# Kernel tuning notes

Hardware: AMD Instinct MI355X
Metric: run time of the kernel (lower is better)

## Reference

```python
import jax, jax.numpy as jnp
import numpy as np

B, D_IN, E, H, V = 4096, 4096, 2048, 2048, 32000


def setup_inputs() -> dict:
    key = jax.random.key(0)
    ks = jax.random.split(key, 24)
    s = 0.02
    p = lambda k, shape: (jax.random.normal(k, shape, dtype=jnp.float32) * s)
    return {
        "input": jax.random.normal(ks[0], (B, D_IN), dtype=jnp.float32),
        "hidden": jnp.zeros((B, H), dtype=jnp.float32),
        "cell": jnp.zeros((B, H), dtype=jnp.float32),
        # embedding linear (input_size -> emb_size), stored as [in, out]
        "We": p(ks[1], (D_IN, E)), "be": p(ks[2], (E,)),
        # x-to-gate linears (emb -> hidden)
        "Wf": p(ks[3], (E, H)), "bf": p(ks[4], (H,)),
        "Wi": p(ks[5], (E, H)), "bi": p(ks[6], (H,)),
        "Wc": p(ks[7], (E, H)), "bc": p(ks[8], (H,)),
        "Wo": p(ks[9], (E, H)), "bo": p(ks[10], (H,)),
        # hidden-to-gate linears (hidden -> hidden)
        "Uf": p(ks[11], (H, H)), "bhf": p(ks[12], (H,)),
        "Ui": p(ks[13], (H, H)), "bhi": p(ks[14], (H,)),
        "Uc": p(ks[15], (H, H)), "bhc": p(ks[16], (H,)),
        "Uo": p(ks[17], (H, H)), "bho": p(ks[18], (H,)),
        # output head (hidden -> output_size)
        "Wend": p(ks[19], (H, V)), "bend": p(ks[20], (V,)),
    }


def reference(input, hidden, cell,
              We, be, Wf, bf, Wi, bi, Wc, bc, Wo, bo,
              Uf, bhf, Ui, bhi, Uc, bhc, Uo, bho, Wend, bend):
    # embedded = Linear(input)
    emb = input @ We + be                                  # [B, E]
    f = jax.nn.sigmoid(emb @ Wf + bf + hidden @ Uf + bhf)  # forget gate [B, H]
    i = jax.nn.sigmoid(emb @ Wi + bi + hidden @ Ui + bhi)  # input gate
    g = jnp.tanh(emb @ Wc + bc + hidden @ Uc + bhc)        # candidate cell
    new_cell = f * cell + i * g
    o = jax.nn.sigmoid(emb @ Wo + bo + hidden @ Uo + bho)  # output gate
    new_hidden = o * jnp.tanh(new_cell)
    out = jax.nn.log_softmax(new_hidden @ Wend + bend, axis=1)  # [B, V]
    return (out, new_hidden, new_cell)
```

## Files before the change

### kernel.cpp

```cpp
#include <hip/hip_runtime.h>
#include <stdint.h>

#define B_DIM 4096
#define DIN   4096
#define E_DIM 2048
#define H_DIM 2048
#define V_DIM 32000

typedef __attribute__((ext_vector_type(8))) short s8v;
typedef __attribute__((ext_vector_type(4))) float f4v;
typedef __attribute__((ext_vector_type(4))) int   i4v;
typedef __attribute__((ext_vector_type(8))) int   i8v;
typedef __attribute__((ext_vector_type(16))) float f16v;

__device__ __forceinline__ ushort f2bf(float f) {
    union { float f; uint32_t u; } v; v.f = f;
    uint32_t u = v.u;
    return (ushort)((u + 0x7FFFu + ((u >> 16) & 1u)) >> 16);
}

__device__ __forceinline__ uint8_t f2fp8(float x) {
    union { float f; uint32_t u; } v; v.f = x;
    uint8_t sign = (uint8_t)((v.u >> 24) & 0x80u);
    uint32_t a = v.u & 0x7FFFFFFFu;
    if (a >= 0x43E00000u) return sign | 0x7E;
    uint32_t r = a + 0x0007FFFFu + ((a >> 20) & 1u);
    int e = (int)(r >> 23) - 127 + 7;
    if (e <= 0) {
        float s = fabsf(x);
        int q = (int)(s * 512.0f + 0.5f);
        if (q > 7) q = 7;
        return sign | (uint8_t)q;
    }
    uint32_t m = (r >> 20) & 7u;
    uint8_t b = (uint8_t)((e << 3) | m);
    if (b == 0x7F) b = 0x7E;
    return sign | b;
}

__global__ void k_cvt(const float* __restrict__ src, ushort* __restrict__ dst, int n4) {
    int i = blockIdx.x * blockDim.x + threadIdx.x;
    if (i >= n4) return;
    float4 v = *(const float4*)(src + (size_t)i * 4);
    ushort4 o;
    o.x = f2bf(v.x); o.y = f2bf(v.y); o.z = f2bf(v.z); o.w = f2bf(v.w);
    *(ushort4*)(dst + (size_t)i * 4) = o;
}

__global__ void k_cvt_hidden(const float* __restrict__ src, ushort* __restrict__ dst) {
    int i = blockIdx.x * blockDim.x + threadIdx.x;
    int b = i >> 9;
    int c = (i & 511) << 2;
    float4 v = *(const float4*)(src + (size_t)b * H_DIM + c);
    ushort4 o;
    o.x = f2bf(v.x); o.y = f2bf(v.y); o.z = f2bf(v.z); o.w = f2bf(v.w);
    *(ushort4*)(dst + (size_t)b * 4096 + 2048 + c) = o;
}

__global__ void k_transpose_bf16(const float* __restrict__ src, ushort* __restrict__ dst,
                                 int srcCols, int dstStride, int dstRowOff, int dstColOff) {
    __shared__ float tile[32][33];
    int tx = threadIdx.x, ty = threadIdx.y;
    int n0 = blockIdx.x * 32, k0 = blockIdx.y * 32;
#pragma unroll
    for (int i = 0; i < 4; i++)
        tile[ty + 8 * i][tx] = src[(size_t)(k0 + ty + 8 * i) * srcCols + n0 + tx];
    __syncthreads();
#pragma unroll
    for (int i = 0; i < 4; i++) {
        int n = ty + 8 * i;
        dst[(size_t)(dstRowOff + n0 + n) * dstStride + dstColOff + k0 + tx] = f2bf(tile[tx][n]);
    }
}

__global__ void k_transpose_fp8(const float* __restrict__ src, uint8_t* __restrict__ dst,
                                int srcCols, int dstStride) {
    __shared__ float tile[32][33];
    int tx = threadIdx.x, ty = threadIdx.y;
    int n0 = blockIdx.x * 32, k0 = blockIdx.y * 32;
#pragma unroll
    for (int i = 0; i < 4; i++)
        tile[ty + 8 * i][tx] = src[(size_t)(k0 + ty + 8 * i) * srcCols + n0 + tx];
    __syncthreads();
#pragma unroll
    for (int i = 0; i < 4; i++) {
        int n = ty + 8 * i;
        dst[(size_t)(n0 + n) * dstStride + k0 + tx] = f2fp8(tile[tx][n] * 32.0f);
    }
}

__global__ void k_transpose_gate(const float* __restrict__ src, ushort* __restrict__ dst,
                                 int g, int dstColOff) {
    __shared__ float tile[32][33];
    int tx = threadIdx.x, ty = threadIdx.y;
    int n0 = blockIdx.x * 32, k0 = blockIdx.y * 32;
#pragma unroll
    for (int i = 0; i < 4; i++)
        tile[ty + 8 * i][tx] = src[(size_t)(k0 + ty + 8 * i) * H_DIM + n0 + tx];
    __syncthreads();
#pragma unroll
    for (int i = 0; i < 4; i++) {
        int h = n0 + ty + 8 * i;
        int drow = ((h >> 6) << 8) + ((g >> 1) << 7) + (((h >> 4) & 3) << 5) + ((g & 1) << 4) + (h & 15);
        dst[(size_t)drow * 4096 + dstColOff + k0 + tx] = f2bf(tile[tx][ty + 8 * i]);
    }
}

__global__ void k_biaspack(const float* __restrict__ b0, const float* __restrict__ bh0,
                           const float* __restrict__ b1, const float* __restrict__ bh1,
                           const float* __restrict__ b2, const float* __restrict__ bh2,
                           const float* __restrict__ b3, const float* __restrict__ bh3,
                           float* __restrict__ out) {
    int h = blockIdx.x * blockDim.x + threadIdx.x;
    if (h >= H_DIM) return;
    int base = ((h >> 6) << 8) + (((h >> 4) & 3) << 5) + (h & 15);
    out[base]             = b0[h] + bh0[h];
    out[base + 16]        = b1[h] + bh1[h];
    out[base + 128]       = b2[h] + bh2[h];
    out[base + 128 + 16]  = b3[h] + bh3[h];
}

template<int OUT_BF16>
__global__ __launch_bounds__(256, 2)
void k_gemm_bt(const ushort* __restrict__ A, const ushort* __restrict__ Bt,
               void* __restrict__ Cv, const float* __restrict__ bias,
               int M, int N, int K, int lda, int ldb, int ldc) {
    __shared__ __align__(16) ushort ldsA[128 * 64];
    __shared__ __align__(16) ushort ldsB[128 * 64];
    const int t = threadIdx.x;
    const int wid = t >> 6, lane = t & 63;

    int nwg = gridDim.x;
    int bid = blockIdx.x;
    int wg  = (bid & 7) * (nwg >> 3) + (bid >> 3);
    int NT  = N >> 7;
    int mt  = wg / NT, nt = wg - mt * NT;
    int m0  = mt << 7, n0 = nt << 7;

    f4v acc[4][4];
#pragma unroll
    for (int i = 0; i < 4; i++)
#pragma unroll
        for (int j = 0; j < 4; j++) acc[i][j] = (f4v){0.f, 0.f, 0.f, 0.f};

    const int wr = wid >> 1, wc = wid & 1;

    const int kTiles = K >> 6;
    for (int kt = 0; kt < kTiles; ++kt) {
#pragma unroll
        for (int c = 0; c < 4; ++c) {
            int idx = c * 256 + wid * 64 + lane;
            int row = idx >> 3;
            int kb  = (idx & 7) << 4;
            const ushort* gA = A  + (size_t)(m0 + row) * lda + (kt << 6) + (kb >> 1);
            const ushort* gB = Bt + (size_t)(n0 + row) * ldb + (kt << 6) + (kb >> 1);
            char* lA = (char*)ldsA + (size_t)(c * 256 + wid * 64) * 16;
            char* lB = (char*)ldsB + (size_t)(c * 256 + wid * 64) * 16;
            __builtin_amdgcn_global_load_lds((const __attribute__((address_space(1))) void*)gA,
                                             (__attribute__((address_space(3))) void*)lA, 16, 0, 0);
            __builtin_amdgcn_global_load_lds((const __attribute__((address_space(1))) void*)gB,
                                             (__attribute__((address_space(3))) void*)lB, 16, 0, 0);
        }
        __syncthreads();

#pragma unroll
        for (int ks = 0; ks < 2; ++ks) {
            s8v af[4], bfr[4];
#pragma unroll
            for (int m = 0; m < 4; ++m) {
                int r = wr * 64 + m * 16 + (lane & 15);
                int kb = ks * 64 + ((lane >> 4) << 4);
                af[m] = *(const s8v*)((const char*)ldsA + r * 128 + kb);
            }
#pragma unroll
            for (int n = 0; n < 4; ++n) {
                int r = wc * 64 + n * 16 + (lane & 15);
                int kb = ks * 64 + ((lane >> 4) << 4);
                bfr[n] = *(const s8v*)((const char*)ldsB + r * 128 + kb);
            }
#pragma unroll
            for (int m = 0; m < 4; ++m)
#pragma unroll
                for (int n = 0; n < 4; ++n)
                    acc[m][n] = __builtin_amdgcn_mfma_f32_16x16x32_bf16(af[m], bfr[n], acc[m][n], 0, 0, 0);
        }
        __syncthreads();
    }

#pragma unroll
    for (int n = 0; n < 4; ++n) {
        int cg = n0 + wc * 64 + n * 16 + (lane & 15);
        float bv = bias[cg];
#pragma unroll
        for (int m = 0; m < 4; ++m) {
            int rbase = m0 + wr * 64 + m * 16 + ((lane >> 4) << 2);
#pragma unroll
            for (int r = 0; r < 4; ++r) {
                float v = acc[m][n][r] + bv;
                if (OUT_BF16)
                    ((ushort*)Cv)[(size_t)(rbase + r) * ldc + cg] = f2bf(v);
                else
                    ((float*)Cv)[(size_t)(rbase + r) * ldc + cg] = v;
            }
        }
    }
}

template<int EPI>
__global__ __launch_bounds__(512, 2)
void k_gemm256(const ushort* __restrict__ A, const ushort* __restrict__ Bt,
               void* __restrict__ Cv, const float* __restrict__ bias,
               int N, int K, int lda, int ldb, int ldc,
               const float* __restrict__ cell, float* __restrict__ outH,
               float* __restrict__ outC, uint8_t* __restrict__ hidF8,
               float2* __restrict__ partials, int ncb) {
    __shared__ __align__(16) ushort ldsA[2][256 * 64];
    __shared__ __align__(16) ushort ldsB[2][256 * 64];
    const int t = threadIdx.x;
    const int wid = t >> 6, lane = t & 63;
    const int wr = wid >> 2, wc = wid & 3;

    int nwg = gridDim.x, bid = blockIdx.x;
    int wg = (bid & 7) * (nwg >> 3) + (bid >> 3);
    int NT = N >> 8;
    int mt = wg / NT, nt = wg - mt * NT;
    int m0 = mt << 8, n0 = nt << 8;

    int offA[4], offB[4];
#pragma unroll
    for (int cc = 0; cc < 4; ++cc) {
        int idx = cc * 512 + t;
        int row = idx >> 3;
        int col = ((idx & 7) ^ (row & 7)) << 3;
        offA[cc] = (m0 + row) * lda + col;
        offB[cc] = (n0 + row) * ldb + col;
    }

#define GLOAD(GP, LP) __builtin_amdgcn_global_load_lds(                                   \
        (const __attribute__((address_space(1))) void*)(GP),                              \
        (__attribute__((address_space(3))) void*)(LP), 16, 0, 0)
#define STAGE_HA(BUF, KT, H) do {                                                         \
    GLOAD(A + offA[(H)*2]     + ((KT) << 6), &ldsA[BUF][(((H)*2)*512 + (wid<<6)) * 8]);   \
    GLOAD(A + offA[(H)*2 + 1] + ((KT) << 6), &ldsA[BUF][(((H)*2+1)*512 + (wid<<6)) * 8]); \
} while (0)
#define STAGE_HB(BUF, KT, H) do {                                                         \
    GLOAD(Bt + offB[(H)*2]     + ((KT) << 6), &ldsB[BUF][(((H)*2)*512 + (wid<<6)) * 8]);  \
    GLOAD(Bt + offB[(H)*2 + 1] + ((KT) << 6), &ldsB[BUF][(((H)*2+1)*512 + (wid<<6)) * 8]);\
} while (0)

    f4v acc[8][4];
#pragma unroll
    for (int i = 0; i < 8; i++)
#pragma unroll
        for (int j = 0; j < 4; j++) acc[i][j] = (f4v){0.f, 0.f, 0.f, 0.f};

    s8v af[4][2], bfA[2][2], bfB[2][2];
    const int swz = (lane & 7) << 4;
    const int kcol = (lane >> 4) << 4;

#define READ_A(BUF, MH) do {                                                              \
    _Pragma("unroll")                                                                     \
    for (int m_ = 0; m_ < 4; ++m_) {                                                      \
        int row = (MH)*128 + wr*64 + m_*16 + (lane & 15);                                 \
        _Pragma("unroll")                                                                 \
        for (int ks_ = 0; ks_ < 2; ++ks_)                                                 \
            af[m_][ks_] = *(const s8v*)((const char*)&ldsA[BUF][0] + row * 128 +          \
                                        ((ks_*64 + kcol) ^ swz));                         \
    } } while (0)
#define READ_B(BUF, NH, DST) do {                                                         \
    _Pragma("unroll")                                                                     \
    for (int n_ = 0; n_ < 2; ++n_) {                                                      \
        int row = (NH)*128 + wc*32 + n_*16 + (lane & 15);                                 \
        _Pragma("unroll")                                                                 \
        for (int ks_ = 0; ks_ < 2; ++ks_)                                                 \
            DST[n_][ks_] = *(const s8v*)((const char*)&ldsB[BUF][0] + row * 128 +         \
                                         ((ks_*64 + kcol) ^ swz));                        \
    } } while (0)
#define MFMA_Q(MH, NH, BF) do {                                                           \
    __builtin_amdgcn_s_setprio(1);                                                        \
    _Pragma("unroll")                                                                     \
    for (int m_ = 0; m_ < 4; ++m_)                                                        \
    _Pragma("unroll")                                                                     \
    for (int n_ = 0; n_ < 2; ++n_)                                                        \
    _Pragma("unroll")                                                                     \
    for (int ks_ = 0; ks_ < 2; ++ks_)                                                     \
        acc[(MH)*4 + m_][(NH)*2 + n_] = __builtin_amdgcn_mfma_f32_16x16x32_bf16(          \
            af[m_][ks_], BF[n_][ks_], acc[(MH)*4 + m_][(NH)*2 + n_], 0, 0, 0);            \
    __builtin_amdgcn_s_setprio(0);                                                        \
} while (0)
#define MEMBAR asm volatile("" ::: "memory")
#define BAR() do { MEMBAR; __builtin_amdgcn_s_barrier(); MEMBAR; } while (0)
#define WAITLGKM0() do { asm volatile("s_waitcnt lgkmcnt(0)" ::: "memory");               \
                         __builtin_amdgcn_sched_barrier(0); } while (0)

    const int kTiles = K >> 6;
    STAGE_HA(0, 0, 0); STAGE_HB(0, 0, 0); STAGE_HB(0, 0, 1); STAGE_HA(0, 0, 1);
    STAGE_HA(1, 1, 0); STAGE_HB(1, 1, 0); STAGE_HB(1, 1, 1); STAGE_HA(1, 1, 1);
    asm volatile("s_waitcnt vmcnt(6)" ::: "memory");
    BAR();

    for (int kt = 0; kt < kTiles; ++kt) {
        const int buf = kt & 1;
        const bool pf = (kt + 2 < kTiles);
        READ_A(buf, 0); READ_B(buf, 0, bfA);
        asm volatile("s_waitcnt lgkmcnt(8)" ::: "memory");
        BAR(); WAITLGKM0();
        MFMA_Q(0, 0, bfA);
        BAR();
        READ_B(buf, 1, bfB);
        if (pf) STAGE_HA(buf, kt + 2, 0);
        BAR(); WAITLGKM0();
        MFMA_Q(0, 1, bfB);
        BAR();
        READ_A(buf, 1);
        if (pf) STAGE_HB(buf, kt + 2, 0);
        BAR(); WAITLGKM0();
        MFMA_Q(1, 1, bfB);
        BAR();
        if (pf) { STAGE_HB(buf, kt + 2, 1); STAGE_HA(buf, kt + 2, 1); }
        MFMA_Q(1, 0, bfA);
        if (pf) asm volatile("s_waitcnt vmcnt(8)" ::: "memory");
        else    asm volatile("s_waitcnt vmcnt(0)" ::: "memory");
        BAR();
    }

    if (EPI == 0) {
    } else {
        int h = (n0 >> 2) + wc * 16 + (lane & 15);
        float bv[4];
#pragma unroll
        for (int j = 0; j < 4; ++j)
            bv[j] = bias[n0 + (j >> 1) * 128 + wc * 32 + (j & 1) * 16 + (lane & 15)];
#pragma unroll
        for (int mh = 0; mh < 2; ++mh)
#pragma unroll
        for (int m = 0; m < 4; ++m) {
            int rb = m0 + mh * 128 + wr * 64 + m * 16 + ((lane >> 4) << 2);
#pragma unroll
            for (int r = 0; r < 4; ++r) {
                int b = rb + r;
                float pf_ = acc[mh * 4 + m][0][r] + bv[0];
                float pi_ = acc[mh * 4 + m][1][r] + bv[1];
                float pc_ = acc[mh * 4 + m][2][r] + bv[2];
                float po_ = acc[mh * 4 + m][3][r] + bv[3];
                float fg = 1.f / (1.f + __expf(-pf_));
                float ig = 1.f / (1.f + __expf(-pi_));
                float gg = tanhf(pc_);
                float og = 1.f / (1.f + __expf(-po_));
                size_t off = (size_t)b * H_DIM + h;
                float nc = fg * cell[off] + ig * gg;
                float nh = og * tanhf(nc);
                outC[off] = nc;
                outH[off] = nh;
                hidF8[off] = f2fp8(nh * 8.0f);
            }
        }
    }
#undef GLOAD
#undef STAGE_HA
#undef STAGE_HB
#undef READ_A
#undef READ_B
#undef MFMA_Q
#undef MEMBAR
#undef BAR
#undef WAITLGKM0
}

__global__ __launch_bounds__(256, 3)
void k_gemm_mx(const uint8_t* __restrict__ A, const uint8_t* __restrict__ Bt,
               float* __restrict__ C, const float* __restrict__ bias,
               float2* __restrict__ partials, int N, int K, int ldc, int ncb) {
    __shared__ __align__(16) uint8_t ldsA[128 * 128];
    __shared__ __align__(16) uint8_t ldsB[128 * 128];
    const int t = threadIdx.x;
    const int wid = t >> 6, lane = t & 63;
    const int wrr = wid >> 1, wcc = wid & 1;

    int nwg = gridDim.x, bid = blockIdx.x;
    int wg = (bid & 7) * (nwg >> 3) + (bid >> 3);
    int NT = N >> 7;
    int mt = wg / NT, nt = wg - mt * NT;
    int m0 = mt << 7, n0 = nt << 7;

    int offA[4], offB[4];
#pragma unroll
    for (int c = 0; c < 4; ++c) {
        int idx = c * 256 + t;
        int row = idx >> 3;
        int cb  = ((idx & 7) ^ (row & 7)) << 4;
        offA[c] = (m0 + row) * K + cb;
        offB[c] = (n0 + row) * K + cb;
    }

    f16v acc[2][2];
#pragma unroll
    for (int i = 0; i < 2; ++i)
#pragma unroll
        for (int j = 0; j < 2; ++j)
#pragma unroll
            for (int r = 0; r < 16; ++r) acc[i][j][r] = 0.f;

    const int lr32 = lane & 31;
    const int kh   = (lane >> 5) << 5;

    const int kTiles = K >> 7;
    for (int kt = 0; kt < kTiles; ++kt) {
#pragma unroll
        for (int c = 0; c < 4; ++c) {
            __builtin_amdgcn_global_load_lds(
                (const __attribute__((address_space(1))) void*)(A + offA[c] + (kt << 7)),
                (__attribute__((address_space(3))) void*)&ldsA[(c * 256 + wid * 64) * 16], 16, 0, 0);
            __builtin_amdgcn_global_load_lds(
                (const __attribute__((address_space(1))) void*)(Bt + offB[c] + (kt << 7)),
                (__attribute__((address_space(3))) void*)&ldsB[(c * 256 + wid * 64) * 16], 16, 0, 0);
        }
        __syncthreads();

#pragma unroll
        for (int kk = 0; kk < 2; ++kk) {
            i8v af[2], bf[2];
#pragma unroll
            for (int mi = 0; mi < 2; ++mi) {
                int row = wrr * 64 + mi * 32 + lr32;
                int sw = (row & 7) << 4;
                int o0 = (kk * 64 + kh) ^ sw;
                int o1 = (kk * 64 + kh + 16) ^ sw;
                i4v lo = *(const i4v*)&ldsA[row * 128 + o0];
                i4v hi = *(const i4v*)&ldsA[row * 128 + o1];
                af[mi] = __builtin_shufflevector(lo, hi, 0, 1, 2, 3, 4, 5, 6, 7);
            }
#pragma unroll
            for (int ni = 0; ni < 2; ++ni) {
                int row = wcc * 64 + ni * 32 + lr32;
                int sw = (row & 7) << 4;
                int o0 = (kk * 64 + kh) ^ sw;
                int o1 = (kk * 64 + kh + 16) ^ sw;
                i4v lo = *(const i4v*)&ldsB[row * 128 + o0];
                i4v hi = *(const i4v*)&ldsB[row * 128 + o1];
                bf[ni] = __builtin_shufflevector(lo, hi, 0, 1, 2, 3, 4, 5, 6, 7);
            }
#pragma unroll
            for (int mi = 0; mi < 2; ++mi)
#pragma unroll
                for (int ni = 0; ni < 2; ++ni)
                    acc[mi][ni] = __builtin_amdgcn_mfma_scale_f32_32x32x64_f8f6f4(
                        af[mi], bf[ni], acc[mi][ni], 0, 0, 0, 124, 0, 122);
        }
        __syncthreads();
    }

    float bv[2];
    int cg0 = n0 + wcc * 64 + lr32;
    bv[0] = bias[cg0];
    bv[1] = bias[cg0 + 32];
    float2* sm = (float2*)ldsA;
#pragma unroll
    for (int mi = 0; mi < 2; ++mi) {
#pragma unroll
        for (int r = 0; r < 16; ++r) {
            int lr = wrr * 64 + mi * 32 + (r & 3) + 8 * (r >> 2) + 4 * (lane >> 5);
            float v0 = acc[mi][0][r] + bv[0];
            float v1 = acc[mi][1][r] + bv[1];
            size_t cr = (size_t)(m0 + lr) * ldc;
            C[cr + cg0] = v0;
            C[cr + cg0 + 32] = v1;
            float mx = fmaxf(v0, v1);
            float ss = __expf(v0 - mx) + __expf(v1 - mx);
#pragma unroll
            for (int off = 1; off < 32; off <<= 1) {
                float mo = __shfl_xor(mx, off);
                float so = __shfl_xor(ss, off);
                float nm = fmaxf(mx, mo);
                ss = ss * __expf(mx - nm) + so * __expf(mo - nm);
                mx = nm;
            }
            if (lr32 == 0) sm[wcc * 128 + lr] = make_float2(mx, ss);
        }
    }
    __syncthreads();
    if (t < 128) {
        float2 a = sm[t], b = sm[128 + t];
        float M = fmaxf(a.x, b.x);
        float S = a.y * __expf(a.x - M) + b.y * __expf(b.x - M);
        partials[(size_t)(m0 + t) * ncb + (n0 >> 7)] = make_float2(M, S);
    }
}

__global__ void k_lsefin(const float2* __restrict__ part, float* __restrict__ lse, int ncb) {
    int row = blockIdx.x;
    int l = threadIdx.x;
    float M = -1e30f, S = 0.f;
    for (int i = l; i < ncb; i += 64) {
        float2 p = part[(size_t)row * ncb + i];
        float nm = fmaxf(M, p.x);
        S = S * __expf(M - nm) + p.y * __expf(p.x - nm);
        M = nm;
    }
#pragma unroll
    for (int off = 1; off < 64; off <<= 1) {
        float Mo = __shfl_xor(M, off);
        float So = __shfl_xor(S, off);
        float nm = fmaxf(M, Mo);
        S = S * __expf(M - nm) + So * __expf(Mo - nm);
        M = nm;
    }
    if (l == 0) lse[row] = M + logf(S);
}

__global__ void k_norm(float* __restrict__ out, const float* __restrict__ lse) {
    int i = blockIdx.x * blockDim.x + threadIdx.x;
    int b = i / (V_DIM / 4);
    int c = (i - b * (V_DIM / 4)) * 4;
    float l = lse[b];
    float* p = out + (size_t)b * V_DIM + c;
    float4 v = *(const float4*)p;
    v.x -= l; v.y -= l; v.z -= l; v.w -= l;
    *(float4*)p = v;
}

extern "C" void kernel_launch(void* const* d_in, const int* in_sizes, int n_in,
                              void* d_out, int out_size, void* d_ws, size_t ws_size,
                              hipStream_t stream) {
    const float* in_input  = (const float*)d_in[0];
    const float* in_hidden = (const float*)d_in[1];
    const float* in_cell   = (const float*)d_in[2];
    const float* We   = (const float*)d_in[3];
    const float* be   = (const float*)d_in[4];
    const float* Wf   = (const float*)d_in[5];
    const float* bfv  = (const float*)d_in[6];
    const float* Wi   = (const float*)d_in[7];
    const float* biv  = (const float*)d_in[8];
    const float* Wc   = (const float*)d_in[9];
    const float* bcv  = (const float*)d_in[10];
    const float* Wo   = (const float*)d_in[11];
    const float* bov  = (const float*)d_in[12];
    const float* Uf   = (const float*)d_in[13];
    const float* bhf  = (const float*)d_in[14];
    const float* Ui   = (const float*)d_in[15];
    const float* bhi  = (const float*)d_in[16];
    const float* Uc   = (const float*)d_in[17];
    const float* bhc  = (const float*)d_in[18];
    const float* Uo   = (const float*)d_in[19];
    const float* bho  = (const float*)d_in[20];
    const float* Wend = (const float*)d_in[21];
    const float* bend = (const float*)d_in[22];

    char* ws = (char*)d_ws;
    const size_t oWendF8 = 0;
    const size_t oHidF8  = oWendF8 + (size_t)V_DIM * H_DIM;
    const size_t oBias2  = oHidF8 + (size_t)B_DIM * H_DIM;
    const size_t oLse    = oBias2 + 4 * H_DIM * 4;
    const size_t oPart   = oLse + B_DIM * 4;
    const size_t oAin    = oPart + (size_t)B_DIM * 250 * 8;
    const size_t oWeT    = oAin + (size_t)B_DIM * DIN * 2;
    const size_t oA2     = oWeT + (size_t)E_DIM * DIN * 2;
    const size_t oWUT    = oA2  + (size_t)B_DIM * 4096 * 2;

    uint8_t* WendF8 = (uint8_t*)(ws + oWendF8);
    uint8_t* hidF8  = (uint8_t*)(ws + oHidF8);
    float*   bias2  = (float*)(ws + oBias2);
    float*   lse    = (float*)(ws + oLse);
    float2*  part   = (float2*)(ws + oPart);
    ushort*  Ain    = (ushort*)(ws + oAin);
    ushort*  WeT    = (ushort*)(ws + oWeT);
    ushort*  A2     = (ushort*)(ws + oA2);
    ushort*  WUT    = (ushort*)(ws + oWUT);

    float* out  = (float*)d_out;
    float* outH = out + (size_t)B_DIM * V_DIM;
    float* outC = outH + (size_t)B_DIM * H_DIM;

    const int NCB = V_DIM / 128;

    dim3 blk256(256), blk512(512), blk64(64);

    k_cvt<<<dim3((B_DIM * DIN / 4) / 256), blk256, 0, stream>>>(in_input, Ain, B_DIM * DIN / 4);
    k_cvt_hidden<<<dim3((B_DIM * H_DIM / 4) / 256), blk256, 0, stream>>>(in_hidden, A2);

    dim3 tb(32, 8);
    k_transpose_bf16<<<dim3(E_DIM / 32, DIN / 32), tb, 0, stream>>>(We, WeT, E_DIM, DIN, 0, 0);
    k_transpose_gate<<<dim3(H_DIM / 32, E_DIM / 32), tb, 0, stream>>>(Wf, WUT, 0, 0);
    k_transpose_gate<<<dim3(H_DIM / 32, E_DIM / 32), tb, 0, stream>>>(Wi, WUT, 1, 0);
    k_transpose_gate<<<dim3(H_DIM / 32, E_DIM / 32), tb, 0, stream>>>(Wc, WUT, 2, 0);
    k_transpose_gate<<<dim3(H_DIM / 32, E_DIM / 32), tb, 0, stream>>>(Wo, WUT, 3, 0);
    k_transpose_gate<<<dim3(H_DIM / 32, H_DIM / 32), tb, 0, stream>>>(Uf, WUT, 0, 2048);
    k_transpose_gate<<<dim3(H_DIM / 32, H_DIM / 32), tb, 0, stream>>>(Ui, WUT, 1, 2048);
    k_transpose_gate<<<dim3(H_DIM / 32, H_DIM / 32), tb, 0, stream>>>(Uc, WUT, 2, 2048);
    k_transpose_gate<<<dim3(H_DIM / 32, H_DIM / 32), tb, 0, stream>>>(Uo, WUT, 3, 2048);
    k_transpose_fp8<<<dim3(V_DIM / 32, H_DIM / 32), tb, 0, stream>>>(Wend, WendF8, V_DIM, H_DIM);
    k_biaspack<<<dim3(H_DIM / 256), blk256, 0, stream>>>(bfv, bhf, biv, bhi, bcv, bhc, bov, bho, bias2);

    k_gemm_bt<1><<<dim3((B_DIM / 128) * (E_DIM / 128)), blk256, 0, stream>>>(
        Ain, WeT, A2, be, B_DIM, E_DIM, DIN, DIN, DIN, 4096);

    k_gemm256<2><<<dim3((B_DIM / 256) * (8192 / 256)), blk512, 0, stream>>>(
        A2, WUT, nullptr, bias2, 8192, 4096, 4096, 4096, 0,
        in_cell, outH, outC, hidF8, nullptr, 0);

    k_gemm_mx<<<dim3((B_DIM / 128) * (V_DIM / 128)), blk256, 0, stream>>>(
        hidF8, WendF8, out, bend, part, V_DIM, H_DIM, V_DIM, NCB);

    k_lsefin<<<dim3(B_DIM), blk64, 0, stream>>>(part, lse, NCB);
    k_norm<<<dim3(B_DIM * (V_DIM / 4) / 256), blk256, 0, stream>>>(out, lse);
}
```

Baseline: 1.219 ms.

## Store head logits as bf16 scratch, switch to 16x16x128 MFMA, M-fastest tile order

The output-head GEMM now writes bf16 logits with nontemporal stores to a scratch buffer that reuses the input-conversion workspace, and the normalization pass reads that bf16 and writes the final fp32 log-softmax. This replaces one fp32 write plus fp32 read-modify-write with a bf16 write, a bf16 read and a single fp32 write. The MFMA changes from 32x32x64 to 16x16x128 with a 4x4 accumulator grid per wave. The tile mapping is hardcoded so that M tiles vary fastest and Wend tiles are reused across CTAs. Logits lose precision to bf16 before the LSE subtraction, and the tile mapping now depends on the fixed grid size.

```diff
diff --git a/kernel.cpp b/kernel.cpp
--- a/kernel.cpp
+++ b/kernel.cpp
@@ -11,12 +11,17 @@
 typedef __attribute__((ext_vector_type(4))) float f4v;
 typedef __attribute__((ext_vector_type(4))) int   i4v;
 typedef __attribute__((ext_vector_type(8))) int   i8v;
-typedef __attribute__((ext_vector_type(16))) float f16v;
+typedef __attribute__((ext_vector_type(4))) uint  u4v;
+typedef __attribute__((ext_vector_type(4))) float f4n;
 
 __device__ __forceinline__ ushort f2bf(float f) {
     union { float f; uint32_t u; } v; v.f = f;
     uint32_t u = v.u;
     return (ushort)((u + 0x7FFFu + ((u >> 16) & 1u)) >> 16);
+}
+__device__ __forceinline__ float bf2f(ushort h) {
+    union { uint32_t u; float f; } v; v.u = ((uint32_t)h) << 16;
+    return v.f;
 }
 
 __device__ __forceinline__ uint8_t f2fp8(float x) {
@@ -369,7 +374,7 @@
 
 __global__ __launch_bounds__(256, 3)
 void k_gemm_mx(const uint8_t* __restrict__ A, const uint8_t* __restrict__ Bt,
-               float* __restrict__ C, const float* __restrict__ bias,
+               ushort* __restrict__ Lbf, const float* __restrict__ bias,
                float2* __restrict__ partials, int N, int K, int ldc, int ncb) {
     __shared__ __align__(16) uint8_t ldsA[128 * 128];
     __shared__ __align__(16) uint8_t ldsB[128 * 128];
@@ -377,11 +382,11 @@
     const int wid = t >> 6, lane = t & 63;
     const int wrr = wid >> 1, wcc = wid & 1;
 
-    int nwg = gridDim.x, bid = blockIdx.x;
-    int wg = (bid & 7) * (nwg >> 3) + (bid >> 3);
-    int NT = N >> 7;
-    int mt = wg / NT, nt = wg - mt * NT;
-    int m0 = mt << 7, n0 = nt << 7;
+    int bid = blockIdx.x;
+    int wg  = (bid & 7) * 1000 + (bid >> 3);
+    int nt  = wg >> 5;
+    int mt  = wg & 31;
+    int m0  = mt << 7, n0 = nt << 7;
 
     int offA[4], offB[4];
 #pragma unroll
@@ -393,16 +398,16 @@
         offB[c] = (n0 + row) * K + cb;
     }
 
-    f16v acc[2][2];
-#pragma unroll
-    for (int i = 0; i < 2; ++i)
-#pragma unroll
-        for (int j = 0; j < 2; ++j)
-#pragma unroll
-            for (int r = 0; r < 16; ++r) acc[i][j][r] = 0.f;
-
-    const int lr32 = lane & 31;
-    const int kh   = (lane >> 5) << 5;
+    f4v acc[4][4];
+#pragma unroll
+    for (int i = 0; i < 4; ++i)
+#pragma unroll
+        for (int j = 0; j < 4; ++j) acc[i][j] = (f4v){0.f, 0.f, 0.f, 0.f};
+
+    const int l15 = lane & 15;
+    const int sw  = (lane & 7) << 4;
+    const int o0  = ((lane >> 4) << 5) ^ sw;
+    const int o1  = o0 ^ 16;
 
     const int kTiles = K >> 7;
     for (int kt = 0; kt < kTiles; ++kt) {
@@ -417,65 +422,59 @@
         }
         __syncthreads();
 
-#pragma unroll
-        for (int kk = 0; kk < 2; ++kk) {
-            i8v af[2], bf[2];
-#pragma unroll
-            for (int mi = 0; mi < 2; ++mi) {
-                int row = wrr * 64 + mi * 32 + lr32;
-                int sw = (row & 7) << 4;
-                int o0 = (kk * 64 + kh) ^ sw;
-                int o1 = (kk * 64 + kh + 16) ^ sw;
-                i4v lo = *(const i4v*)&ldsA[row * 128 + o0];
-                i4v hi = *(const i4v*)&ldsA[row * 128 + o1];
-                af[mi] = __builtin_shufflevector(lo, hi, 0, 1, 2, 3, 4, 5, 6, 7);
-            }
-#pragma unroll
-            for (int ni = 0; ni < 2; ++ni) {
-                int row = wcc * 64 + ni * 32 + lr32;
-                int sw = (row & 7) << 4;
-                int o0 = (kk * 64 + kh) ^ sw;
-                int o1 = (kk * 64 + kh + 16) ^ sw;
-                i4v lo = *(const i4v*)&ldsB[row * 128 + o0];
-                i4v hi = *(const i4v*)&ldsB[row * 128 + o1];
-                bf[ni] = __builtin_shufflevector(lo, hi, 0, 1, 2, 3, 4, 5, 6, 7);
-            }
-#pragma unroll
-            for (int mi = 0; mi < 2; ++mi)
-#pragma unroll
-                for (int ni = 0; ni < 2; ++ni)
-                    acc[mi][ni] = __builtin_amdgcn_mfma_scale_f32_32x32x64_f8f6f4(
-                        af[mi], bf[ni], acc[mi][ni], 0, 0, 0, 124, 0, 122);
-        }
+        i8v af[4], bf[4];
+#pragma unroll
+        for (int m = 0; m < 4; ++m) {
+            int row = wrr * 64 + m * 16 + l15;
+            i4v lo = *(const i4v*)&ldsA[row * 128 + o0];
+            i4v hi = *(const i4v*)&ldsA[row * 128 + o1];
+            af[m] = __builtin_shufflevector(lo, hi, 0, 1, 2, 3, 4, 5, 6, 7);
+        }
+#pragma unroll
+        for (int n = 0; n < 4; ++n) {
+            int row = wcc * 64 + n * 16 + l15;
+            i4v lo = *(const i4v*)&ldsB[row * 128 + o0];
+            i4v hi = *(const i4v*)&ldsB[row * 128 + o1];
+            bf[n] = __builtin_shufflevector(lo, hi, 0, 1, 2, 3, 4, 5, 6, 7);
+        }
+#pragma unroll
+        for (int m = 0; m < 4; ++m)
+#pragma unroll
+            for (int n = 0; n < 4; ++n)
+                acc[m][n] = __builtin_amdgcn_mfma_scale_f32_16x16x128_f8f6f4(
+                    af[m], bf[n], acc[m][n], 0, 0, 0, 124, 0, 122);
         __syncthreads();
     }
 
-    float bv[2];
-    int cg0 = n0 + wcc * 64 + lr32;
-    bv[0] = bias[cg0];
-    bv[1] = bias[cg0 + 32];
+    float bv[4];
+#pragma unroll
+    for (int n = 0; n < 4; ++n) bv[n] = bias[n0 + wcc * 64 + n * 16 + l15];
     float2* sm = (float2*)ldsA;
 #pragma unroll
-    for (int mi = 0; mi < 2; ++mi) {
-#pragma unroll
-        for (int r = 0; r < 16; ++r) {
-            int lr = wrr * 64 + mi * 32 + (r & 3) + 8 * (r >> 2) + 4 * (lane >> 5);
-            float v0 = acc[mi][0][r] + bv[0];
-            float v1 = acc[mi][1][r] + bv[1];
-            size_t cr = (size_t)(m0 + lr) * ldc;
-            C[cr + cg0] = v0;
-            C[cr + cg0 + 32] = v1;
-            float mx = fmaxf(v0, v1);
-            float ss = __expf(v0 - mx) + __expf(v1 - mx);
-#pragma unroll
-            for (int off = 1; off < 32; off <<= 1) {
+    for (int m = 0; m < 4; ++m) {
+#pragma unroll
+        for (int r = 0; r < 4; ++r) {
+            int rl = wrr * 64 + m * 16 + ((lane >> 4) << 2) + r;
+            float v[4];
+#pragma unroll
+            for (int n = 0; n < 4; ++n) v[n] = acc[m][n][r] + bv[n];
+            size_t cr = (size_t)(m0 + rl) * ldc + n0 + wcc * 64 + l15;
+            __builtin_nontemporal_store(f2bf(v[0]), &Lbf[cr]);
+            __builtin_nontemporal_store(f2bf(v[1]), &Lbf[cr + 16]);
+            __builtin_nontemporal_store(f2bf(v[2]), &Lbf[cr + 32]);
+            __builtin_nontemporal_store(f2bf(v[3]), &Lbf[cr + 48]);
+            float mx = fmaxf(fmaxf(v[0], v[1]), fmaxf(v[2], v[3]));
+            float ss = __expf(v[0] - mx) + __expf(v[1] - mx) +
+                       __expf(v[2] - mx) + __expf(v[3] - mx);
+#pragma unroll
+            for (int off = 1; off < 16; off <<= 1) {
                 float mo = __shfl_xor(mx, off);
                 float so = __shfl_xor(ss, off);
                 float nm = fmaxf(mx, mo);
                 ss = ss * __expf(mx - nm) + so * __expf(mo - nm);
                 mx = nm;
             }
-            if (lr32 == 0) sm[wcc * 128 + lr] = make_float2(mx, ss);
+            if (l15 == 0) sm[wcc * 128 + rl] = make_float2(mx, ss);
         }
     }
     __syncthreads();
@@ -483,7 +482,7 @@
         float2 a = sm[t], b = sm[128 + t];
         float M = fmaxf(a.x, b.x);
         float S = a.y * __expf(a.x - M) + b.y * __expf(b.x - M);
-        partials[(size_t)(m0 + t) * ncb + (n0 >> 7)] = make_float2(M, S);
+        partials[(size_t)(m0 + t) * ncb + nt] = make_float2(M, S);
     }
 }
 
@@ -508,15 +507,26 @@
     if (l == 0) lse[row] = M + logf(S);
 }
 
-__global__ void k_norm(float* __restrict__ out, const float* __restrict__ lse) {
-    int i = blockIdx.x * blockDim.x + threadIdx.x;
-    int b = i / (V_DIM / 4);
-    int c = (i - b * (V_DIM / 4)) * 4;
+__global__ void k_norm(const ushort* __restrict__ Lbf, const float* __restrict__ lse,
+                       float* __restrict__ out) {
+    int b = blockIdx.y;
+    int c8 = blockIdx.x * blockDim.x + threadIdx.x;
+    if (c8 >= V_DIM / 8) return;
     float l = lse[b];
-    float* p = out + (size_t)b * V_DIM + c;
-    float4 v = *(const float4*)p;
-    v.x -= l; v.y -= l; v.z -= l; v.w -= l;
-    *(float4*)p = v;
+    const u4v* src = (const u4v*)(Lbf + (size_t)b * V_DIM + (size_t)c8 * 8);
+    u4v pv = __builtin_nontemporal_load(src);
+    f4n q0, q1;
+    q0.x = bf2f((ushort)(pv.x & 0xFFFF)) - l;
+    q0.y = bf2f((ushort)(pv.x >> 16)) - l;
+    q0.z = bf2f((ushort)(pv.y & 0xFFFF)) - l;
+    q0.w = bf2f((ushort)(pv.y >> 16)) - l;
+    q1.x = bf2f((ushort)(pv.z & 0xFFFF)) - l;
+    q1.y = bf2f((ushort)(pv.z >> 16)) - l;
+    q1.z = bf2f((ushort)(pv.w & 0xFFFF)) - l;
+    q1.w = bf2f((ushort)(pv.w >> 16)) - l;
+    float* dst = out + (size_t)b * V_DIM + (size_t)c8 * 8;
+    __builtin_nontemporal_store(q0, (f4n*)dst);
+    __builtin_nontemporal_store(q1, (f4n*)(dst + 4));
 }
 
 extern "C" void kernel_launch(void* const* d_in, const int* in_sizes, int n_in,
@@ -552,7 +562,8 @@
     const size_t oBias2  = oHidF8 + (size_t)B_DIM * H_DIM;
     const size_t oLse    = oBias2 + 4 * H_DIM * 4;
     const size_t oPart   = oLse + B_DIM * 4;
-    const size_t oAin    = oPart + (size_t)B_DIM * 250 * 8;
+    const size_t oR      = oPart + (size_t)B_DIM * 250 * 8;
+    const size_t oAin    = oR;
     const size_t oWeT    = oAin + (size_t)B_DIM * DIN * 2;
     const size_t oA2     = oWeT + (size_t)E_DIM * DIN * 2;
     const size_t oWUT    = oA2  + (size_t)B_DIM * 4096 * 2;
@@ -562,6 +573,7 @@
     float*   bias2  = (float*)(ws + oBias2);
     float*   lse    = (float*)(ws + oLse);
     float2*  part   = (float2*)(ws + oPart);
+    ushort*  Lbf    = (ushort*)(ws + oR);
     ushort*  Ain    = (ushort*)(ws + oAin);
     ushort*  WeT    = (ushort*)(ws + oWeT);
     ushort*  A2     = (ushort*)(ws + oA2);
@@ -599,8 +611,8 @@
         in_cell, outH, outC, hidF8, nullptr, 0);
 
     k_gemm_mx<<<dim3((B_DIM / 128) * (V_DIM / 128)), blk256, 0, stream>>>(
-        hidF8, WendF8, out, bend, part, V_DIM, H_DIM, V_DIM, NCB);
+        hidF8, WendF8, Lbf, bend, part, V_DIM, H_DIM, V_DIM, NCB);
 
     k_lsefin<<<dim3(B_DIM), blk64, 0, stream>>>(part, lse, NCB);
-    k_norm<<<dim3(B_DIM * (V_DIM / 4) / 256), blk256, 0, stream>>>(out, lse);
-}
+    k_norm<<<dim3(16, B_DIM), blk256, 0, stream>>>(Lbf, lse, out);
+}
```

New measurement: 1.244 ms. 2.1% more time.
